# Kernel optimization log

Measured on AMD Instinct MI355X. Metric: run time of the kernel, lower is better.

## Reference

```python
import jax, jax.numpy as jnp
import numpy as np

EMBED_DIM = 384
NUM_HEADS = 8
WINDOW = 8
SHIFT = 4


def setup_inputs() -> dict:
    key = jax.random.key(0)
    ks = jax.random.split(key, 8)
    B, C, H, W = 4, EMBED_DIM, 256, 256
    X_f = jax.random.normal(ks[0], (B, C, H, W), dtype=jnp.float32)
    X_s = jax.random.normal(ks[1], (B, C, H, W), dtype=jnp.float32)
    std = 0.02
    Wq = jax.random.normal(ks[2], (C, C), dtype=jnp.float32) * std
    Wk = jax.random.normal(ks[3], (C, C), dtype=jnp.float32) * std
    Wv = jax.random.normal(ks[4], (C, C), dtype=jnp.float32) * std
    Wo = jax.random.normal(ks[5], (C, C), dtype=jnp.float32) * std
    bq = jnp.zeros((C,), jnp.float32)
    bk = jnp.zeros((C,), jnp.float32)
    bv = jnp.zeros((C,), jnp.float32)
    bo = jnp.zeros((C,), jnp.float32)
    return {"X_f": X_f, "X_s": X_s, "Wq": Wq, "bq": bq, "Wk": Wk, "bk": bk,
            "Wv": Wv, "bv": bv, "Wo": Wo, "bo": bo}


def reference(X_f, X_s, Wq, bq, Wk, bk, Wv, bv, Wo, bo):
    B, C, H, W = X_f.shape
    nh, ws, shift = NUM_HEADS, WINDOW, SHIFT
    hd = C // nh
    scale = hd ** (-0.5)

    # pad spatial features to multiple of window size (no-op here, kept for fidelity)
    pad_h = (ws - H % ws) % ws
    pad_w = (ws - W % ws) % ws
    pt, pb = pad_h // 2, pad_h - pad_h // 2
    pl, pr = pad_w // 2, pad_w - pad_w // 2
    Xs = jnp.pad(X_s, ((0, 0), (0, 0), (pt, pb), (pl, pr)))
    Hp, Wp = H + pad_h, W + pad_w

    # global-pooled frequency query
    Qg = X_f.mean(axis=(2, 3))                      # (B, C)
    Q = (Qg @ Wq.T + bq).reshape(B, nh, hd)         # (B, nh, hd)

    # cyclic shift + channel-last projections for K, V
    sh = jnp.roll(Xs, shift=(shift, shift), axis=(2, 3))
    x = sh.transpose(0, 2, 3, 1)                    # (B, Hp, Wp, C)
    K = x @ Wk.T + bk
    V = x @ Wv.T + bv

    nWh, nWw = Hp // ws, Wp // ws
    nW = nWh * nWw

    def window(t):
        # (B, Hp, Wp, C) -> (B, nW, ws*ws, nh, hd)
        t = t.reshape(B, nWh, ws, nWw, ws, nh, hd)
        return t.transpose(0, 1, 3, 2, 4, 5, 6).reshape(B, nW, ws * ws, nh, hd)

    Kw = window(K)
    Vw = window(V)

    # single-query attention per window
    scores = jnp.einsum('bhd,bwkhd->bwhk', Q, Kw) * scale
    attn = jax.nn.softmax(scores, axis=-1)
    ow = jnp.einsum('bwhk,bwkhd->bwhd', attn, Vw)   # (B, nW, nh, hd)

    out = ow.mean(axis=1).reshape(B, C)             # average over windows
    out = out @ Wo.T + bo
    return jnp.broadcast_to(out[:, :, None, None], (B, C, H, W))
```

## Files before the change

kernel.cpp:

```cpp
#include <hip/hip_runtime.h>
#include <hip/hip_fp16.h>
#include <stdint.h>

namespace {
constexpr int B = 4, C = 384, Wd = 256, HW = 65536;
constexpr int NH = 8, HD = 48, SH = 4;
constexpr float SCALE = 0.14433756729740643f;
constexpr int CH = C / 2;

__global__ __launch_bounds__(256) void k_mean(const float* __restrict__ Xf,
                                              float* __restrict__ Qg) {
  int bc = blockIdx.x;
  const float4* p = reinterpret_cast<const float4*>(Xf + (size_t)bc * HW);
  float s = 0.f;
  for (int it = threadIdx.x; it < HW / 4; it += 256) {
    float4 v = p[it];
    s += (v.x + v.y) + (v.z + v.w);
  }
  __shared__ float red[256];
  red[threadIdx.x] = s;
  __syncthreads();
  for (int off = 128; off > 0; off >>= 1) {
    if (threadIdx.x < off) red[threadIdx.x] += red[threadIdx.x + off];
    __syncthreads();
  }
  if (threadIdx.x == 0) Qg[bc] = red[0] * (1.0f / HW);
}

__global__ __launch_bounds__(256) void k_proj(const float* __restrict__ Qg,
                                              const float* __restrict__ Wq,
                                              const float* __restrict__ bq,
                                              const float* __restrict__ Wk,
                                              float* __restrict__ Qk) {
  __shared__ float Qs[B * C];
  int t = threadIdx.x;
  for (int idx = t; idx < B * C; idx += 256) {
    int b = idx / C, o = idx % C;
    const float* qg = Qg + b * C;
    const float* w = Wq + (size_t)o * C;
    float s = bq[o];
    for (int c = 0; c < C; c++) s += qg[c] * w[c];
    Qs[idx] = s;
  }
  __syncthreads();
  for (int idx = t; idx < B * NH * C; idx += 256) {
    int c = idx % C;
    int bh = idx / C;
    int h = bh % NH, b = bh / NH;
    float s = 0.f;
    for (int d = 0; d < HD; d++)
      s += Qs[b * C + h * HD + d] * Wk[(size_t)(h * HD + d) * C + c];
    Qk[idx] = s;
  }
}

__global__ __launch_bounds__(256) void k_scores(const float* __restrict__ Xs,
                                                const float* __restrict__ Qk,
                                                float* __restrict__ Sp) {
  int x = blockIdx.x;
  int b = x >> 7;
  int rowgrp = (x >> 1) & 63;
  int chalf = x & 1;
  int c0 = chalf * CH;
  float* Spart = Sp + (size_t)chalf * ((size_t)B * NH * HW);

  __shared__ __align__(16) float qk[CH * 8];
  for (int idx = threadIdx.x; idx < CH * 8; idx += 256) {
    int cl = idx >> 3, h = idx & 7;
    qk[idx] = Qk[((size_t)(b * NH + h)) * C + c0 + cl];
  }
  __syncthreads();

  int r = threadIdx.x >> 6;
  int j4 = (threadIdx.x & 63) * 4;
  int si = rowgrp * 4 + r;

  float acc[4][8];
#pragma unroll
  for (int p = 0; p < 4; p++)
#pragma unroll
    for (int h = 0; h < NH; h++) acc[p][h] = 0.f;

  const float* xp = Xs + ((size_t)(b * C + c0)) * HW + si * Wd + j4;
#pragma unroll 4
  for (int cl = 0; cl < CH; cl++) {
    float4 xv = *reinterpret_cast<const float4*>(xp + (size_t)cl * HW);
    float4 q0 = *reinterpret_cast<const float4*>(&qk[cl * 8]);
    float4 q1 = *reinterpret_cast<const float4*>(&qk[cl * 8 + 4]);
    float qv[8] = {q0.x, q0.y, q0.z, q0.w, q1.x, q1.y, q1.z, q1.w};
    float xa[4] = {xv.x, xv.y, xv.z, xv.w};
#pragma unroll
    for (int p = 0; p < 4; p++)
#pragma unroll
      for (int h = 0; h < NH; h++) acc[p][h] += xa[p] * qv[h];
  }

  int i = (si + SH) & 255;
  int js = (j4 + SH) & 255;
#pragma unroll
  for (int h = 0; h < NH; h++) {
    float4 o = make_float4(acc[0][h], acc[1][h], acc[2][h], acc[3][h]);
    *reinterpret_cast<float4*>(Spart + ((size_t)(b * NH + h)) * HW + i * Wd + js) = o;
  }
}

__global__ __launch_bounds__(256) void k_softmax(const float* __restrict__ Sp,
                                                 uint16_t* __restrict__ Wb) {
  const float* S0 = Sp;
  const float* S1 = Sp + (size_t)B * NH * HW;
  int wid = threadIdx.x >> 6, lane = threadIdx.x & 63;
  int gid = blockIdx.x * 4 + wid;
  int b = gid >> 10;
  int w = gid & 1023;
  int i = (w >> 5) * 8 + (lane >> 3);
  int j = (w & 31) * 8 + (lane & 7);

  union { __half h[8]; uint4 u; } pk;
#pragma unroll
  for (int h = 0; h < NH; h++) {
    size_t idx = ((size_t)(b * NH + h)) * HW + i * Wd + j;
    float s = (S0[idx] + S1[idx]) * SCALE;
    float m = s;
#pragma unroll
    for (int o = 32; o > 0; o >>= 1) m = fmaxf(m, __shfl_xor(m, o));
    float e = __expf(s - m);
    float sum = e;
#pragma unroll
    for (int o = 32; o > 0; o >>= 1) sum += __shfl_xor(sum, o);
    pk.h[h] = __float2half(e / sum);
  }
  uint4* dst = reinterpret_cast<uint4*>(Wb) + (size_t)b * HW + i * Wd + j;
  *dst = pk.u;
}

__global__ __launch_bounds__(256) void k_pool(const float* __restrict__ Xs,
                                              const uint16_t* __restrict__ Wb,
                                              float* __restrict__ Y) {
  int bc = blockIdx.x;
  int b = bc / C, c = bc % C;
  int sj = threadIdx.x;
  int jw = (sj + SH) & 255;
  const float* xp = Xs + (size_t)bc * HW + sj;
  const uint4* wp = reinterpret_cast<const uint4*>(Wb) + (size_t)b * HW + jw;

  float acc[8];
#pragma unroll
  for (int h = 0; h < 8; h++) acc[h] = 0.f;

#pragma unroll 2
  for (int si = 0; si < 256; si++) {
    float xv = xp[(size_t)si * Wd];
    int iw = (si + SH) & 255;
    uint4 wv = wp[(size_t)iw * Wd];
    const __half2* h2 = reinterpret_cast<const __half2*>(&wv);
#pragma unroll
    for (int k = 0; k < 4; k++) {
      float2 f = __half22float2(h2[k]);
      acc[2 * k] += xv * f.x;
      acc[2 * k + 1] += xv * f.y;
    }
  }

  __shared__ float red[256];
  for (int h = 0; h < 8; h++) {
    red[threadIdx.x] = acc[h];
    __syncthreads();
    for (int off = 128; off > 0; off >>= 1) {
      if (threadIdx.x < off) red[threadIdx.x] += red[threadIdx.x + off];
      __syncthreads();
    }
    if (threadIdx.x == 0) Y[((size_t)(b * NH + h)) * C + c] = red[0];
    __syncthreads();
  }
}

__global__ __launch_bounds__(384) void k_head(const float* __restrict__ Y,
                                              const float* __restrict__ Wv,
                                              const float* __restrict__ bv,
                                              const float* __restrict__ Wo,
                                              const float* __restrict__ bo,
                                              float* __restrict__ Fin) {
  int b = blockIdx.x;
  int o = threadIdx.x;
  __shared__ float op[C];
  int h = o / HD;
  const float* y = Y + (size_t)(b * NH + h) * C;
  const float* w = Wv + (size_t)o * C;
  float s = 0.f;
  for (int c = 0; c < C; c++) s += w[c] * y[c];
  op[o] = s * (1.0f / 1024.0f) + bv[o];
  __syncthreads();
  const float* w2 = Wo + (size_t)o * C;
  float s2 = bo[o];
  for (int c = 0; c < C; c++) s2 += w2[c] * op[c];
  Fin[b * C + o] = s2;
}

__global__ __launch_bounds__(256) void k_bcast(const float* __restrict__ Fin,
                                               float* __restrict__ Out) {
  int bc = blockIdx.x;
  float v = Fin[bc];
  float4 v4 = make_float4(v, v, v, v);
  float4* op = reinterpret_cast<float4*>(Out + (size_t)bc * HW);
  for (int it = threadIdx.x; it < HW / 4; it += 256) op[it] = v4;
}

}

extern "C" void kernel_launch(void* const* d_in, const int* in_sizes, int n_in,
                              void* d_out, int out_size, void* d_ws, size_t ws_size,
                              hipStream_t stream) {
  const float* Xf = (const float*)d_in[0];
  const float* Xs = (const float*)d_in[1];
  const float* Wq = (const float*)d_in[2];
  const float* bq = (const float*)d_in[3];
  const float* Wk = (const float*)d_in[4];
  const float* Wv = (const float*)d_in[6];
  const float* bv = (const float*)d_in[7];
  const float* Wo = (const float*)d_in[8];
  const float* bo = (const float*)d_in[9];
  float* Out = (float*)d_out;

  char* ws = (char*)d_ws;
  uint16_t* Wb = (uint16_t*)(ws);
  float* Sp = (float*)(ws + ((size_t)4 << 20));
  char* tail = ws + ((size_t)20 << 20);
  float* Qg = (float*)(tail);
  float* Qk = (float*)(tail + 6144);
  float* Y = (float*)(tail + 6144 + 49152);
  float* Fin = (float*)(tail + 6144 + 49152 + 49152);

  k_mean<<<B * C, 256, 0, stream>>>(Xf, Qg);
  k_proj<<<1, 256, 0, stream>>>(Qg, Wq, bq, Wk, Qk);
  k_scores<<<512, 256, 0, stream>>>(Xs, Qk, Sp);
  k_softmax<<<1024, 256, 0, stream>>>(Sp, Wb);
  k_pool<<<B * C, 256, 0, stream>>>(Xs, Wb, Y);
  k_head<<<B, 384, 0, stream>>>(Y, Wv, bv, Wo, bo, Fin);
  k_bcast<<<B * C, 256, 0, stream>>>(Fin, Out);
}
```

Baseline: 1.229 ms.

## Fuse scores, softmax and pooling into one per-window attention kernel

Replaces the three kernels (scores into a partial-sum buffer, softmax into fp16 weights, pooling that rereads X_s) with a single per-window kernel. Each block loads its 8x8 window across all channels once, keeps a half-precision copy in shared memory, computes the scores, runs the softmax, and does the weighted pooling from shared memory. The goal is to read X_s from HBM once instead of twice and to avoid the global score and weight buffers. In exchange it adds fp16 rounding of X in the pooling step and many float atomicAdds into Y, which now has to be zeroed in k_proj.

Result: faster. 1.167 ms (-5.1%).

```diff
diff --git a/kernel.cpp b/kernel.cpp
--- a/kernel.cpp
+++ b/kernel.cpp
@@ -6,7 +6,6 @@
 constexpr int B = 4, C = 384, Wd = 256, HW = 65536;
 constexpr int NH = 8, HD = 48, SH = 4;
 constexpr float SCALE = 0.14433756729740643f;
-constexpr int CH = C / 2;
 
 __global__ __launch_bounds__(256) void k_mean(const float* __restrict__ Xf,
                                               float* __restrict__ Qg) {
@@ -31,9 +30,11 @@
                                               const float* __restrict__ Wq,
                                               const float* __restrict__ bq,
                                               const float* __restrict__ Wk,
-                                              float* __restrict__ Qk) {
+                                              float* __restrict__ Qk,
+                                              float* __restrict__ Y) {
+  int t = threadIdx.x;
+  for (int i = t; i < B * NH * C; i += 256) Y[i] = 0.f;
   __shared__ float Qs[B * C];
-  int t = threadIdx.x;
   for (int idx = t; idx < B * C; idx += 256) {
     int b = idx / C, o = idx % C;
     const float* qg = Qg + b * C;
@@ -50,127 +51,124 @@
     float s = 0.f;
     for (int d = 0; d < HD; d++)
       s += Qs[b * C + h * HD + d] * Wk[(size_t)(h * HD + d) * C + c];
-    Qk[idx] = s;
-  }
-}
-
-__global__ __launch_bounds__(256) void k_scores(const float* __restrict__ Xs,
-                                                const float* __restrict__ Qk,
-                                                float* __restrict__ Sp) {
-  int x = blockIdx.x;
-  int b = x >> 7;
-  int rowgrp = (x >> 1) & 63;
-  int chalf = x & 1;
-  int c0 = chalf * CH;
-  float* Spart = Sp + (size_t)chalf * ((size_t)B * NH * HW);
-
-  __shared__ __align__(16) float qk[CH * 8];
-  for (int idx = threadIdx.x; idx < CH * 8; idx += 256) {
-    int cl = idx >> 3, h = idx & 7;
-    qk[idx] = Qk[((size_t)(b * NH + h)) * C + c0 + cl];
-  }
-  __syncthreads();
-
-  int r = threadIdx.x >> 6;
-  int j4 = (threadIdx.x & 63) * 4;
-  int si = rowgrp * 4 + r;
-
-  float acc[4][8];
-#pragma unroll
-  for (int p = 0; p < 4; p++)
-#pragma unroll
-    for (int h = 0; h < NH; h++) acc[p][h] = 0.f;
-
-  const float* xp = Xs + ((size_t)(b * C + c0)) * HW + si * Wd + j4;
+    Qk[((size_t)b * C + c) * NH + h] = s;
+  }
+}
+
+__global__ __launch_bounds__(256) void k_attn(const float* __restrict__ Xs,
+                                              const float* __restrict__ Qk,
+                                              float* __restrict__ Y) {
+  __shared__ __align__(16) __half Xh[C][66];
+  __shared__ __align__(16) float Qks[C][8];
+  __shared__ __align__(16) float Sred[4][16][33];
+  __shared__ __align__(16) float Wl[64][12];
+
+  int raw = blockIdx.x;
+  int bw = (raw & 7) * 512 + (raw >> 3);
+  int b = bw >> 10, w = bw & 1023;
+  int wi = w >> 5, wj = w & 31;
+  int t = threadIdx.x;
+
+  {
+    const float4* src = reinterpret_cast<const float4*>(Qk + (size_t)b * C * NH);
+    float4* dst = reinterpret_cast<float4*>(&Qks[0][0]);
+    for (int i = t; i < C * NH / 4; i += 256) dst[i] = src[i];
+  }
+  __syncthreads();
+
+  int q = t & 15, g = t >> 4;
+  int r = q >> 1, jq = q & 1;
+  int si = ((wi << 3) + r + 256 - SH) & 255;
+  int sj = ((wj << 3) + (jq << 2) + 256 - SH) & 255;
+  const float* xb = Xs + (((size_t)b * C + g) << 16) + si * Wd + sj;
+
+  float sp[4][8];
+#pragma unroll
+  for (int e = 0; e < 4; e++)
+#pragma unroll
+    for (int h = 0; h < 8; h++) sp[e][h] = 0.f;
+
 #pragma unroll 4
-  for (int cl = 0; cl < CH; cl++) {
-    float4 xv = *reinterpret_cast<const float4*>(xp + (size_t)cl * HW);
-    float4 q0 = *reinterpret_cast<const float4*>(&qk[cl * 8]);
-    float4 q1 = *reinterpret_cast<const float4*>(&qk[cl * 8 + 4]);
-    float qv[8] = {q0.x, q0.y, q0.z, q0.w, q1.x, q1.y, q1.z, q1.w};
+  for (int k = 0; k < 24; k++) {
+    int c = g + (k << 4);
+    float4 xv = *reinterpret_cast<const float4*>(xb + ((size_t)(k << 4) << 16));
+    const float4* qp = reinterpret_cast<const float4*>(&Qks[c][0]);
+    float4 qa = qp[0], qb = qp[1];
+    __half2 h01 = __float22half2_rn(make_float2(xv.x, xv.y));
+    __half2 h23 = __float22half2_rn(make_float2(xv.z, xv.w));
+    __half2* xw = reinterpret_cast<__half2*>(&Xh[c][q << 2]);
+    xw[0] = h01;
+    xw[1] = h23;
     float xa[4] = {xv.x, xv.y, xv.z, xv.w};
 #pragma unroll
-    for (int p = 0; p < 4; p++)
-#pragma unroll
-      for (int h = 0; h < NH; h++) acc[p][h] += xa[p] * qv[h];
-  }
-
-  int i = (si + SH) & 255;
-  int js = (j4 + SH) & 255;
-#pragma unroll
-  for (int h = 0; h < NH; h++) {
-    float4 o = make_float4(acc[0][h], acc[1][h], acc[2][h], acc[3][h]);
-    *reinterpret_cast<float4*>(Spart + ((size_t)(b * NH + h)) * HW + i * Wd + js) = o;
-  }
-}
-
-__global__ __launch_bounds__(256) void k_softmax(const float* __restrict__ Sp,
-                                                 uint16_t* __restrict__ Wb) {
-  const float* S0 = Sp;
-  const float* S1 = Sp + (size_t)B * NH * HW;
-  int wid = threadIdx.x >> 6, lane = threadIdx.x & 63;
-  int gid = blockIdx.x * 4 + wid;
-  int b = gid >> 10;
-  int w = gid & 1023;
-  int i = (w >> 5) * 8 + (lane >> 3);
-  int j = (w & 31) * 8 + (lane & 7);
-
-  union { __half h[8]; uint4 u; } pk;
-#pragma unroll
-  for (int h = 0; h < NH; h++) {
-    size_t idx = ((size_t)(b * NH + h)) * HW + i * Wd + j;
-    float s = (S0[idx] + S1[idx]) * SCALE;
+    for (int e = 0; e < 4; e++) {
+      sp[e][0] += xa[e] * qa.x; sp[e][1] += xa[e] * qa.y;
+      sp[e][2] += xa[e] * qa.z; sp[e][3] += xa[e] * qa.w;
+      sp[e][4] += xa[e] * qb.x; sp[e][5] += xa[e] * qb.y;
+      sp[e][6] += xa[e] * qb.z; sp[e][7] += xa[e] * qb.w;
+    }
+  }
+
+#pragma unroll
+  for (int e = 0; e < 4; e++)
+#pragma unroll
+    for (int h = 0; h < 8; h++) {
+      float v = sp[e][h];
+      v += __shfl_xor(v, 16);
+      v += __shfl_xor(v, 32);
+      sp[e][h] = v;
+    }
+  int wv = t >> 6;
+  int gg = g & 3;
+#pragma unroll
+  for (int h = 0; h < 8; h++) {
+    float v = (gg == 0) ? sp[0][h] : (gg == 1) ? sp[1][h] : (gg == 2) ? sp[2][h] : sp[3][h];
+    Sred[wv][q][gg * 8 + h] = v;
+  }
+  __syncthreads();
+
+  int p = t & 63, hg = t >> 6;
+  int qq = p >> 2, ee = p & 3;
+#pragma unroll
+  for (int hh = 0; hh < 2; hh++) {
+    int h = hg * 2 + hh;
+    float s = Sred[0][qq][ee * 8 + h] + Sred[1][qq][ee * 8 + h] +
+              Sred[2][qq][ee * 8 + h] + Sred[3][qq][ee * 8 + h];
+    s *= SCALE;
     float m = s;
 #pragma unroll
-    for (int o = 32; o > 0; o >>= 1) m = fmaxf(m, __shfl_xor(m, o));
+    for (int off = 32; off > 0; off >>= 1) m = fmaxf(m, __shfl_xor(m, off));
     float e = __expf(s - m);
     float sum = e;
 #pragma unroll
-    for (int o = 32; o > 0; o >>= 1) sum += __shfl_xor(sum, o);
-    pk.h[h] = __float2half(e / sum);
-  }
-  uint4* dst = reinterpret_cast<uint4*>(Wb) + (size_t)b * HW + i * Wd + j;
-  *dst = pk.u;
-}
-
-__global__ __launch_bounds__(256) void k_pool(const float* __restrict__ Xs,
-                                              const uint16_t* __restrict__ Wb,
-                                              float* __restrict__ Y) {
-  int bc = blockIdx.x;
-  int b = bc / C, c = bc % C;
-  int sj = threadIdx.x;
-  int jw = (sj + SH) & 255;
-  const float* xp = Xs + (size_t)bc * HW + sj;
-  const uint4* wp = reinterpret_cast<const uint4*>(Wb) + (size_t)b * HW + jw;
-
-  float acc[8];
-#pragma unroll
-  for (int h = 0; h < 8; h++) acc[h] = 0.f;
-
-#pragma unroll 2
-  for (int si = 0; si < 256; si++) {
-    float xv = xp[(size_t)si * Wd];
-    int iw = (si + SH) & 255;
-    uint4 wv = wp[(size_t)iw * Wd];
-    const __half2* h2 = reinterpret_cast<const __half2*>(&wv);
-#pragma unroll
-    for (int k = 0; k < 4; k++) {
-      float2 f = __half22float2(h2[k]);
-      acc[2 * k] += xv * f.x;
-      acc[2 * k + 1] += xv * f.y;
+    for (int off = 32; off > 0; off >>= 1) sum += __shfl_xor(sum, off);
+    Wl[p][h] = e / sum;
+  }
+  __syncthreads();
+
+  for (int c = t; c < C; c += 256) {
+    float acc[8];
+#pragma unroll
+    for (int h = 0; h < 8; h++) acc[h] = 0.f;
+    const __half2* xr = reinterpret_cast<const __half2*>(&Xh[c][0]);
+#pragma unroll 4
+    for (int p4 = 0; p4 < 16; p4++) {
+      float2 x01 = __half22float2(xr[p4 * 2]);
+      float2 x23 = __half22float2(xr[p4 * 2 + 1]);
+      float xa[4] = {x01.x, x01.y, x23.x, x23.y};
+#pragma unroll
+      for (int e = 0; e < 4; e++) {
+        const float4* wr = reinterpret_cast<const float4*>(&Wl[p4 * 4 + e][0]);
+        float4 w0 = wr[0], w1 = wr[1];
+        acc[0] += xa[e] * w0.x; acc[1] += xa[e] * w0.y;
+        acc[2] += xa[e] * w0.z; acc[3] += xa[e] * w0.w;
+        acc[4] += xa[e] * w1.x; acc[5] += xa[e] * w1.y;
+        acc[6] += xa[e] * w1.z; acc[7] += xa[e] * w1.w;
+      }
     }
-  }
-
-  __shared__ float red[256];
-  for (int h = 0; h < 8; h++) {
-    red[threadIdx.x] = acc[h];
-    __syncthreads();
-    for (int off = 128; off > 0; off >>= 1) {
-      if (threadIdx.x < off) red[threadIdx.x] += red[threadIdx.x + off];
-      __syncthreads();
-    }
-    if (threadIdx.x == 0) Y[((size_t)(b * NH + h)) * C + c] = red[0];
-    __syncthreads();
+    float* yp = Y + (size_t)b * NH * C;
+#pragma unroll
+    for (int h = 0; h < 8; h++) atomicAdd(&yp[h * C + c], acc[h]);
   }
 }
 
@@ -222,19 +220,14 @@
   float* Out = (float*)d_out;
 
   char* ws = (char*)d_ws;
-  uint16_t* Wb = (uint16_t*)(ws);
-  float* Sp = (float*)(ws + ((size_t)4 << 20));
-  char* tail = ws + ((size_t)20 << 20);
-  float* Qg = (float*)(tail);
-  float* Qk = (float*)(tail + 6144);
-  float* Y = (float*)(tail + 6144 + 49152);
-  float* Fin = (float*)(tail + 6144 + 49152 + 49152);
+  float* Qg = (float*)(ws);
+  float* Qk = (float*)(ws + 8192);
+  float* Y  = (float*)(ws + 8192 + 65536);
+  float* Fin = (float*)(ws + 8192 + 131072);
 
   k_mean<<<B * C, 256, 0, stream>>>(Xf, Qg);
-  k_proj<<<1, 256, 0, stream>>>(Qg, Wq, bq, Wk, Qk);
-  k_scores<<<512, 256, 0, stream>>>(Xs, Qk, Sp);
-  k_softmax<<<1024, 256, 0, stream>>>(Sp, Wb);
-  k_pool<<<B * C, 256, 0, stream>>>(Xs, Wb, Y);
+  k_proj<<<1, 256, 0, stream>>>(Qg, Wq, bq, Wk, Qk, Y);
+  k_attn<<<B * 1024, 256, 0, stream>>>(Xs, Qk, Y);
   k_head<<<B, 384, 0, stream>>>(Y, Wv, bv, Wo, bo, Fin);
   k_bcast<<<B * C, 256, 0, stream>>>(Fin, Out);
 }
```
